# Kernel tuning notes

Hardware: AMD Instinct MI355X
Metric: run time of the kernel (lower is better)

## Reference

```python
import jax, jax.numpy as jnp
import numpy as np

NEG_INF = -1e10  # matches torch masked_fill value -10000000000.0


def setup_inputs() -> dict:
    key = jax.random.key(0)
    k1, k2, k3, k4 = jax.random.split(key, 4)
    B, Lq, Lk, D = 8, 2048, 2048, 1024
    hidden = jax.random.normal(k1, (B, Lq, D), dtype=jnp.float32)
    keys = jax.random.normal(k2, (B, Lk, D), dtype=jnp.float32)
    values = jax.random.normal(k3, (B, Lk, D), dtype=jnp.float32)
    mask = jax.random.randint(k4, (B, Lk), 0, 2, dtype=jnp.int32)
    return {"hidden": hidden, "keys": keys, "values": values, "mask": mask}


def reference(hidden, keys, values, mask):
    # scores[b,q,k] = sum_d hidden[b,q,d] * keys[b,k,d]  (unscaled dot-product)
    scores = jnp.einsum("bqd,bkd->bqk", hidden, keys)
    scores = jnp.where(mask[:, None, :] == 0, NEG_INF, scores)
    weights = jax.nn.softmax(scores, axis=2)  # (B, Lq, Lk)
    # context[b,q,d] = sum_k weights[b,q,k] * values[b,k,d]
    context = jnp.einsum("bqk,bkd->bqd", weights, values)
    return context
```

## Files before the change

### kernel.cpp

```cpp
#include <hip/hip_runtime.h>

#define NEG_INF -1e10f
#define B_   8
#define LQ_  2048
#define LK_  2048
#define D_   1024

typedef unsigned int uint;
typedef unsigned short u16;
typedef _Float16 f16;
typedef _Float16 f16x8_t __attribute__((ext_vector_type(8)));
typedef float f32x4_t __attribute__((ext_vector_type(4)));

__device__ __forceinline__ u16 f2h_bits(float f) {
    f16 h = (f16)f;
    return __builtin_bit_cast(u16, h);
}
__device__ __forceinline__ void gload_lds16(const void* g, void* l) {
    __builtin_amdgcn_global_load_lds(
        (const __attribute__((address_space(1))) uint*)g,
        (__attribute__((address_space(3))) uint*)l, 16, 0, 0);
}

__global__ __launch_bounds__(256) void convert_f16(
    const float4* __restrict__ src, ushort4* __restrict__ dst, int n4)
{
    int idx = blockIdx.x * 256 + threadIdx.x;
    const int stride = gridDim.x * 256;
    for (; idx < n4; idx += stride) {
        float4 x = src[idx];
        ushort4 h;
        h.x = f2h_bits(x.x);
        h.y = f2h_bits(x.y);
        h.z = f2h_bits(x.z);
        h.w = f2h_bits(x.w);
        dst[idx] = h;
    }
}

__global__ __launch_bounds__(256) void transpose_convert(
    const float* __restrict__ V, u16* __restrict__ VT)
{
    __shared__ float tile[64][65];
    const int t  = threadIdx.x;
    const int d0 = blockIdx.x * 64;
    const int k0 = blockIdx.y * 64;
    const float* Vb = V + (size_t)blockIdx.z * (LK_ * D_);
    u16* VTb = VT + (size_t)blockIdx.z * (D_ * LK_);
#pragma unroll
    for (int i = 0; i < 4; ++i) {
        int f = i * 256 + t;
        int r = f >> 4, c4 = f & 15;
        float4 v = *(const float4*)&Vb[(size_t)(k0 + r) * D_ + d0 + c4 * 4];
        tile[r][c4 * 4 + 0] = v.x;
        tile[r][c4 * 4 + 1] = v.y;
        tile[r][c4 * 4 + 2] = v.z;
        tile[r][c4 * 4 + 3] = v.w;
    }
    __syncthreads();
#pragma unroll
    for (int i = 0; i < 4; ++i) {
        int f = i * 256 + t;
        int d = f >> 4, c4 = f & 15;
        ushort4 o;
        o.x = f2h_bits(tile[c4 * 4 + 0][d]);
        o.y = f2h_bits(tile[c4 * 4 + 1][d]);
        o.z = f2h_bits(tile[c4 * 4 + 2][d]);
        o.w = f2h_bits(tile[c4 * 4 + 3][d]);
        *(ushort4*)&VTb[(size_t)(d0 + d) * LK_ + k0 + c4 * 4] = o;
    }
}

#define BM_  256
#define BK_  32

template<int NBF, int NTILES, bool SPLIT>
__global__ __launch_bounds__(512, 2) void gemm8p(
    const u16* __restrict__ A0g, const u16* __restrict__ A1g,
    const u16* __restrict__ Bg, float* __restrict__ Cg,
    int lda, int ldb, int ldc, int bkmask,
    size_t szA, size_t szB, size_t szC)
{
    constexpr int BN     = 64 * NBF;
    constexpr int ABYTES = BM_ * BK_ * 2;
    constexpr int BBYTES = BN * BK_ * 2;
    constexpr int BUFSZ  = ABYTES + BBYTES;
    __shared__ char lds[4 * BUFSZ];

    const int tid  = threadIdx.x;
    const int lane = tid & 63;
    const int w    = tid >> 6;
    const int wm   = w >> 2;
    const int wn   = w & 3;

    const int d  = blockIdx.x;
    const int g  = d & 7;
    const int k_ = d >> 3;
    const int by = (g >> 1) * 2 + (k_ & 1);
    const int bx = (g & 1) * 4 + (k_ >> 1);
    const int m0 = by * BM_;
    const int n0 = bx * BN;
    const size_t z = blockIdx.y;

    const u16* A0 = A0g + z * szA;
    const u16* A1 = A1g + z * szA;
    const u16* B  = Bg  + z * szB;
    float* C = Cg + z * szC;

    const int  lr   = lane & 15;
    const uint csel = (uint)((((lane >> 4) ^ ((lane >> 1) & 3)) * 16));
    const int  cstg = (((lane & 3) ^ ((lane >> 3) & 3)) * 8);
    const int  rstg = lane >> 2;

    const uint awoff = (uint)(wm * 8192 + lr * 64) + csel;
    const uint bwoff = (uint)(wn * (NBF * 1024) + lr * 64) + csel;

    f32x4_t acc[8][NBF];
#pragma unroll
    for (int m = 0; m < 8; ++m)
#pragma unroll
        for (int n = 0; n < NBF; ++n)
            acc[m][n] = (f32x4_t){0.f, 0.f, 0.f, 0.f};

    auto stA = [&](int t) {
        const u16* Ab;
        int kc;
        if constexpr (SPLIT) {
            Ab = (t < NTILES / 2) ? A0 : A1;
            kc = (t & (NTILES / 2 - 1)) * BK_ + cstg;
        } else {
            Ab = A0;
            kc = t * BK_ + cstg;
        }
        char* dst = lds + (t & 3) * BUFSZ + w * 2048;
        gload_lds16(&Ab[(size_t)(m0 + w * 32 + rstg) * lda + kc], dst);
        gload_lds16(&Ab[(size_t)(m0 + w * 32 + 16 + rstg) * lda + kc], dst + 1024);
    };
    auto stB = [&](int t) {
        const int kc = ((t * BK_) & bkmask) + cstg;
        char* dst = lds + (t & 3) * BUFSZ + ABYTES;
        if constexpr (NBF == 4) {
            gload_lds16(&B[(size_t)(n0 + w * 32 + rstg) * ldb + kc], dst + w * 2048);
            gload_lds16(&B[(size_t)(n0 + w * 32 + 16 + rstg) * ldb + kc], dst + w * 2048 + 1024);
        } else {
            gload_lds16(&B[(size_t)(n0 + w * 16 + rstg) * ldb + kc], dst + w * 1024);
        }
    };

    stA(0); stB(0); stA(1); stB(1); stA(2); stB(2);
    if constexpr (NBF == 4) asm volatile("s_waitcnt vmcnt(8)" ::: "memory");
    else                    asm volatile("s_waitcnt vmcnt(6)" ::: "memory");
    __builtin_amdgcn_s_barrier();

#define LDF(p) (*(const f16x8_t*)(p))

#define PHASE_A(T, DOSTAGE)                                                   \
    {                                                                         \
        const char* pA = lds + ((T) & 3) * BUFSZ + awoff;                     \
        const char* pB = lds + ((T) & 3) * BUFSZ + ABYTES + bwoff;            \
        f16x8_t a[4], b[NBF];                                                 \
        a[0] = LDF(pA);        a[1] = LDF(pA + 1024);                         \
        a[2] = LDF(pA + 2048); a[3] = LDF(pA + 3072);                         \
        b[0] = LDF(pB);                                                       \
        if constexpr (NBF >= 2) b[1] = LDF(pB + 1024);                        \
        if constexpr (NBF == 4) { b[2] = LDF(pB + 2048); b[3] = LDF(pB + 3072); } \
        if (DOSTAGE) stA((T) + 3);                                            \
        __builtin_amdgcn_s_barrier();                                         \
        __builtin_amdgcn_s_setprio(1);                                        \
        _Pragma("unroll")                                                     \
        for (int mf = 0; mf < 4; ++mf)                                        \
            _Pragma("unroll")                                                 \
            for (int nf = 0; nf < NBF; ++nf)                                  \
                acc[mf][nf] = __builtin_amdgcn_mfma_f32_16x16x32_f16(         \
                    a[mf], b[nf], acc[mf][nf], 0, 0, 0);                      \
        __builtin_amdgcn_s_setprio(0);                                        \
        bsave[0] = b[0];                                                      \
        if constexpr (NBF >= 2) bsave[1] = b[1];                              \
        if constexpr (NBF == 4) { bsave[2] = b[2]; bsave[3] = b[3]; }         \
        __builtin_amdgcn_s_barrier();                                         \
    }

#define PHASE_B(T, DOSTAGE, VMASM)                                            \
    {                                                                         \
        const char* pA = lds + ((T) & 3) * BUFSZ + awoff;                     \
        f16x8_t a[4];                                                         \
        a[0] = LDF(pA + 4096); a[1] = LDF(pA + 5120);                         \
        a[2] = LDF(pA + 6144); a[3] = LDF(pA + 7168);                         \
        if (DOSTAGE) stB((T) + 3);                                            \
        __builtin_amdgcn_s_barrier();                                         \
        __builtin_amdgcn_s_setprio(1);                                        \
        _Pragma("unroll")                                                     \
        for (int mf = 0; mf < 4; ++mf)                                        \
            _Pragma("unroll")                                                 \
            for (int nf = 0; nf < NBF; ++nf)                                  \
                acc[4 + mf][nf] = __builtin_amdgcn_mfma_f32_16x16x32_f16(     \
                    a[mf], bsave[nf], acc[4 + mf][nf], 0, 0, 0);              \
        __builtin_amdgcn_s_setprio(0);                                        \
        VMASM;                                                                \
        __builtin_amdgcn_s_barrier();                                         \
    }

#define VMW do { if constexpr (NBF == 4) asm volatile("s_waitcnt vmcnt(8)" ::: "memory"); \
                 else asm volatile("s_waitcnt vmcnt(6)" ::: "memory"); } while (0)
#define VMH do { if constexpr (NBF == 4) asm volatile("s_waitcnt vmcnt(4)" ::: "memory"); \
                 else asm volatile("s_waitcnt vmcnt(3)" ::: "memory"); } while (0)
#define VM0 asm volatile("s_waitcnt vmcnt(0)" ::: "memory")
#define VMN do {} while (0)

    f16x8_t bsave[NBF];

    for (int t = 0; t < NTILES - 3; ++t) {
        PHASE_A(t, true);
        PHASE_B(t, true, VMW);
    }
    PHASE_A(NTILES - 3, false); PHASE_B(NTILES - 3, false, VMH);
    PHASE_A(NTILES - 2, false); PHASE_B(NTILES - 2, false, VM0);
    PHASE_A(NTILES - 1, false); PHASE_B(NTILES - 1, false, VMN);
#undef PHASE_A
#undef PHASE_B
#undef LDF

    const int cg = lane >> 4;
#pragma unroll
    for (int mf = 0; mf < 8; ++mf)
#pragma unroll
        for (int nf = 0; nf < NBF; ++nf) {
            const int row = m0 + wm * 128 + mf * 16 + cg * 4;
            const int col = n0 + wn * (NBF * 16) + nf * 16 + lr;
#pragma unroll
            for (int r = 0; r < 4; ++r)
                C[(size_t)(row + r) * ldc + col] = acc[mf][nf][r];
        }
}

__global__ __launch_bounds__(256) void softmax_mask(
    float* __restrict__ S, const int* __restrict__ mask0)
{
    const int lane = threadIdx.x & 63;
    const int wave = threadIdx.x >> 6;
    const int row  = blockIdx.x * 4 + wave;
    const size_t zb = blockIdx.y;
    float* Sr = S + (zb * LQ_ + row) * (size_t)LK_;
    const int* mb = mask0 + zb * LK_;

    float4 s[8];
    float m = -INFINITY;
#pragma unroll
    for (int i = 0; i < 8; ++i) {
        int k = i * 256 + lane * 4;
        float4 v = *(const float4*)&Sr[k];
        int4 mk  = *(const int4*)&mb[k];
        v.x = mk.x ? v.x : NEG_INF;
        v.y = mk.y ? v.y : NEG_INF;
        v.z = mk.z ? v.z : NEG_INF;
        v.w = mk.w ? v.w : NEG_INF;
        s[i] = v;
        m = fmaxf(m, fmaxf(fmaxf(v.x, v.y), fmaxf(v.z, v.w)));
    }
#pragma unroll
    for (int off = 32; off > 0; off >>= 1)
        m = fmaxf(m, __shfl_xor(m, off, 64));
    float sum = 0.f;
#pragma unroll
    for (int i = 0; i < 8; ++i) {
        s[i].x = __expf(s[i].x - m); sum += s[i].x;
        s[i].y = __expf(s[i].y - m); sum += s[i].y;
        s[i].z = __expf(s[i].z - m); sum += s[i].z;
        s[i].w = __expf(s[i].w - m); sum += s[i].w;
    }
#pragma unroll
    for (int off = 32; off > 0; off >>= 1)
        sum += __shfl_xor(sum, off, 64);
    const float inv = 1.f / sum;
    u16* Pr = (u16*)Sr;
#pragma unroll
    for (int i = 0; i < 8; ++i) {
        int k = i * 256 + lane * 4;
        ushort4 o;
        o.x = f2h_bits(s[i].x * inv);
        o.y = f2h_bits(s[i].y * inv);
        o.z = f2h_bits(s[i].z * inv);
        o.w = f2h_bits(s[i].w * inv);
        *(ushort4*)&Pr[k] = o;
    }
}

__global__ __launch_bounds__(256, 2) void attn_fp32_flash(
    const float* __restrict__ hidden, const float* __restrict__ keys,
    const float* __restrict__ values, const int* __restrict__ mask,
    float* __restrict__ out)
{
    const int lane = threadIdx.x & 63;
    const int wave = threadIdx.x >> 6;
    const int blk  = blockIdx.x;
    const int b    = blk >> 7;
    const int q0   = (blk & 127) * 16 + wave * 4;
    float4 q[4][4]; float4 o[4][4]; float m[4], s[4];
    const float4* hp = (const float4*)(hidden + ((size_t)b * LQ_ + q0) * D_);
#pragma unroll
    for (int r = 0; r < 4; ++r) {
#pragma unroll
        for (int j = 0; j < 4; ++j) {
            q[r][j] = hp[r * 256 + j * 64 + lane];
            o[r][j] = make_float4(0.f, 0.f, 0.f, 0.f);
        }
        m[r] = -INFINITY; s[r] = 0.f;
    }
    const float4* kp = (const float4*)(keys   + (size_t)b * LK_ * D_);
    const float4* vp = (const float4*)(values + (size_t)b * LK_ * D_);
    const int*    mp = mask + b * LK_;
    for (int k = 0; k < LK_; ++k) {
        float4 kv[4];
#pragma unroll
        for (int j = 0; j < 4; ++j) kv[j] = kp[k * 256 + j * 64 + lane];
        float sc[4];
#pragma unroll
        for (int r = 0; r < 4; ++r) {
            float p = 0.f;
#pragma unroll
            for (int j = 0; j < 4; ++j)
                p += q[r][j].x * kv[j].x + q[r][j].y * kv[j].y +
                     q[r][j].z * kv[j].z + q[r][j].w * kv[j].w;
            sc[r] = p;
        }
#pragma unroll
        for (int r = 0; r < 4; ++r)
#pragma unroll
            for (int off = 32; off > 0; off >>= 1)
                sc[r] += __shfl_xor(sc[r], off, 64);
        const int mk = mp[k];
        float4 vv[4];
#pragma unroll
        for (int j = 0; j < 4; ++j) vv[j] = vp[k * 256 + j * 64 + lane];
#pragma unroll
        for (int r = 0; r < 4; ++r) {
            float score = mk ? sc[r] : NEG_INF;
            if (score > m[r]) {
                float scale = __expf(m[r] - score);
                m[r] = score; s[r] *= scale;
#pragma unroll
                for (int j = 0; j < 4; ++j) {
                    o[r][j].x *= scale; o[r][j].y *= scale;
                    o[r][j].z *= scale; o[r][j].w *= scale;
                }
            }
            float e = __expf(score - m[r]);
            s[r] += e;
#pragma unroll
            for (int j = 0; j < 4; ++j) {
                o[r][j].x += e * vv[j].x; o[r][j].y += e * vv[j].y;
                o[r][j].z += e * vv[j].z; o[r][j].w += e * vv[j].w;
            }
        }
    }
    float4* op = (float4*)(out + ((size_t)b * LQ_ + q0) * D_);
#pragma unroll
    for (int r = 0; r < 4; ++r) {
        float inv = 1.f / s[r];
#pragma unroll
        for (int j = 0; j < 4; ++j) {
            float4 t = o[r][j];
            t.x *= inv; t.y *= inv; t.z *= inv; t.w *= inv;
            op[r * 256 + j * 64 + lane] = t;
        }
    }
}

extern "C" void kernel_launch(void* const* d_in, const int* in_sizes, int n_in,
                              void* d_out, int out_size, void* d_ws, size_t ws_size,
                              hipStream_t stream) {
    const float* hidden = (const float*)d_in[0];
    const float* keys   = (const float*)d_in[1];
    const float* values = (const float*)d_in[2];
    const int*   mask   = (const int*)d_in[3];
    float* out = (float*)d_out;
    char* ws = (char*)d_ws;

    const size_t TEN = (size_t)LK_ * D_;
    const size_t MB  = 1024ull * 1024;

    int BG = 0;
    for (int g = 8; g >= 1; g >>= 1)
        if ((size_t)g * 28 * MB <= ws_size) { BG = g; break; }

    if (BG == 0) {
        attn_fp32_flash<<<1024, 256, 0, stream>>>(hidden, keys, values, mask, out);
        return;
    }

    const size_t SZ_BF = (size_t)BG * TEN * 2;
    u16*   Kh = (u16*)(ws);
    u16*   VT = (u16*)(ws + SZ_BF);
    u16*   Qh = (u16*)(ws + 2 * SZ_BF);
    float* S  = (float*)(ws + 3 * SZ_BF);

    const int n4 = BG * (int)(TEN / 4);

    for (int bg0 = 0; bg0 < B_; bg0 += BG) {
        const size_t off = (size_t)bg0 * TEN;
        convert_f16<<<2048, 256, 0, stream>>>(
            (const float4*)(keys + off), (ushort4*)Kh, n4);
        transpose_convert<<<dim3(16, 32, BG), 256, 0, stream>>>(
            values + off, VT);
        convert_f16<<<2048, 256, 0, stream>>>(
            (const float4*)(hidden + off), (ushort4*)Qh, n4);

        gemm8p<4, 32, false><<<dim3(64, BG), 512, 0, stream>>>(
            Qh, Qh, Kh, S, D_, D_, LK_, 1023,
            TEN, TEN, (size_t)LQ_ * LK_);

        softmax_mask<<<dim3(LQ_ / 4, BG), 256, 0, stream>>>(
            S, mask + bg0 * LK_);

        gemm8p<2, 64, true><<<dim3(64, BG), 512, 0, stream>>>(
            (const u16*)S, (const u16*)S + 1024, VT, out + off,
            2 * LK_, LK_, D_, 2047,
            (size_t)LQ_ * 2 * LK_, TEN, (size_t)LQ_ * D_);
    }
}
```

Measured before the change: 257.8 us.

## Widen PV GEMM tile to 256 columns and merge Q/K conversion launches

The second GEMM (weights times V^T) now uses NBF=4, giving 256-wide N tiles with 32 blocks per batch instead of 64, and the tile mapping for the split variant is adjusted to match. Each block reuses its A tile (the softmax weights) across more output columns, cutting LDS and global traffic for A. The two fp32-to-fp16 conversions for keys and hidden are fused into one launch to save a kernel launch. The trade-off is fewer blocks per batch, which lowers occupancy and parallelism on the GPU, and higher register use for accumulators.

After: 238.9 us. -7.3%, faster.

```diff
diff --git a/kernel.cpp b/kernel.cpp
--- a/kernel.cpp
+++ b/kernel.cpp
@@ -22,19 +22,22 @@
         (__attribute__((address_space(3))) uint*)l, 16, 0, 0);
 }
 
-__global__ __launch_bounds__(256) void convert_f16(
-    const float4* __restrict__ src, ushort4* __restrict__ dst, int n4)
+__global__ __launch_bounds__(256) void convert_f16_2(
+    const float4* __restrict__ s1, ushort4* __restrict__ d1,
+    const float4* __restrict__ s2, ushort4* __restrict__ d2, int n4)
 {
     int idx = blockIdx.x * 256 + threadIdx.x;
     const int stride = gridDim.x * 256;
-    for (; idx < n4; idx += stride) {
-        float4 x = src[idx];
+    for (; idx < 2 * n4; idx += stride) {
+        const bool second = idx >= n4;
+        const int i = second ? idx - n4 : idx;
+        float4 x = second ? s2[i] : s1[i];
         ushort4 h;
         h.x = f2h_bits(x.x);
         h.y = f2h_bits(x.y);
         h.z = f2h_bits(x.z);
         h.w = f2h_bits(x.w);
-        dst[idx] = h;
+        if (second) d2[i] = h; else d1[i] = h;
     }
 }
 
@@ -96,8 +99,14 @@
     const int d  = blockIdx.x;
     const int g  = d & 7;
     const int k_ = d >> 3;
-    const int by = (g >> 1) * 2 + (k_ & 1);
-    const int bx = (g & 1) * 4 + (k_ >> 1);
+    int by, bx;
+    if constexpr (!SPLIT) {
+        by = (g >> 1) * 2 + (k_ & 1);
+        bx = (g & 1) * 4 + (k_ >> 1);
+    } else {
+        by = (g >> 1) * 2 + (k_ & 1);
+        bx = (g & 1) * 2 + (k_ >> 1);
+    }
     const int m0 = by * BM_;
     const int n0 = bx * BN;
     const size_t z = blockIdx.y;
@@ -139,17 +148,12 @@
     auto stB = [&](int t) {
         const int kc = ((t * BK_) & bkmask) + cstg;
         char* dst = lds + (t & 3) * BUFSZ + ABYTES;
-        if constexpr (NBF == 4) {
-            gload_lds16(&B[(size_t)(n0 + w * 32 + rstg) * ldb + kc], dst + w * 2048);
-            gload_lds16(&B[(size_t)(n0 + w * 32 + 16 + rstg) * ldb + kc], dst + w * 2048 + 1024);
-        } else {
-            gload_lds16(&B[(size_t)(n0 + w * 16 + rstg) * ldb + kc], dst + w * 1024);
-        }
+        gload_lds16(&B[(size_t)(n0 + w * 32 + rstg) * ldb + kc], dst + w * 2048);
+        gload_lds16(&B[(size_t)(n0 + w * 32 + 16 + rstg) * ldb + kc], dst + w * 2048 + 1024);
     };
 
     stA(0); stB(0); stA(1); stB(1); stA(2); stB(2);
-    if constexpr (NBF == 4) asm volatile("s_waitcnt vmcnt(8)" ::: "memory");
-    else                    asm volatile("s_waitcnt vmcnt(6)" ::: "memory");
+    asm volatile("s_waitcnt vmcnt(8)" ::: "memory");
     __builtin_amdgcn_s_barrier();
 
 #define LDF(p) (*(const f16x8_t*)(p))
@@ -161,9 +165,8 @@
         f16x8_t a[4], b[NBF];                                                 \
         a[0] = LDF(pA);        a[1] = LDF(pA + 1024);                         \
         a[2] = LDF(pA + 2048); a[3] = LDF(pA + 3072);                         \
-        b[0] = LDF(pB);                                                       \
-        if constexpr (NBF >= 2) b[1] = LDF(pB + 1024);                        \
-        if constexpr (NBF == 4) { b[2] = LDF(pB + 2048); b[3] = LDF(pB + 3072); } \
+        b[0] = LDF(pB);        b[1] = LDF(pB + 1024);                         \
+        b[2] = LDF(pB + 2048); b[3] = LDF(pB + 3072);                         \
         if (DOSTAGE) stA((T) + 3);                                            \
         __builtin_amdgcn_s_barrier();                                         \
         __builtin_amdgcn_s_setprio(1);                                        \
@@ -174,9 +177,7 @@
                 acc[mf][nf] = __builtin_amdgcn_mfma_f32_16x16x32_f16(         \
                     a[mf], b[nf], acc[mf][nf], 0, 0, 0);                      \
         __builtin_amdgcn_s_setprio(0);                                        \
-        bsave[0] = b[0];                                                      \
-        if constexpr (NBF >= 2) bsave[1] = b[1];                              \
-        if constexpr (NBF == 4) { bsave[2] = b[2]; bsave[3] = b[3]; }         \
+        bsave[0] = b[0]; bsave[1] = b[1]; bsave[2] = b[2]; bsave[3] = b[3];   \
         __builtin_amdgcn_s_barrier();                                         \
     }
 
@@ -200,10 +201,8 @@
         __builtin_amdgcn_s_barrier();                                         \
     }
 
-#define VMW do { if constexpr (NBF == 4) asm volatile("s_waitcnt vmcnt(8)" ::: "memory"); \
-                 else asm volatile("s_waitcnt vmcnt(6)" ::: "memory"); } while (0)
-#define VMH do { if constexpr (NBF == 4) asm volatile("s_waitcnt vmcnt(4)" ::: "memory"); \
-                 else asm volatile("s_waitcnt vmcnt(3)" ::: "memory"); } while (0)
+#define VMW asm volatile("s_waitcnt vmcnt(8)" ::: "memory")
+#define VMH asm volatile("s_waitcnt vmcnt(4)" ::: "memory")
 #define VM0 asm volatile("s_waitcnt vmcnt(0)" ::: "memory")
 #define VMN do {} while (0)
 
@@ -398,12 +397,11 @@
 
     for (int bg0 = 0; bg0 < B_; bg0 += BG) {
         const size_t off = (size_t)bg0 * TEN;
-        convert_f16<<<2048, 256, 0, stream>>>(
-            (const float4*)(keys + off), (ushort4*)Kh, n4);
+        convert_f16_2<<<4096, 256, 0, stream>>>(
+            (const float4*)(keys + off), (ushort4*)Kh,
+            (const float4*)(hidden + off), (ushort4*)Qh, n4);
         transpose_convert<<<dim3(16, 32, BG), 256, 0, stream>>>(
             values + off, VT);
-        convert_f16<<<2048, 256, 0, stream>>>(
-            (const float4*)(hidden + off), (ushort4*)Qh, n4);
 
         gemm8p<4, 32, false><<<dim3(64, BG), 512, 0, stream>>>(
             Qh, Qh, Kh, S, D_, D_, LK_, 1023,
@@ -412,7 +410,7 @@
         softmax_mask<<<dim3(LQ_ / 4, BG), 256, 0, stream>>>(
             S, mask + bg0 * LK_);
 
-        gemm8p<2, 64, true><<<dim3(64, BG), 512, 0, stream>>>(
+        gemm8p<4, 64, true><<<dim3(32, BG), 512, 0, stream>>>(
             (const u16*)S, (const u16*)S + 1024, VT, out + off,
             2 * LK_, LK_, D_, 2047,
             (size_t)LQ_ * 2 * LK_, TEN, (size_t)LQ_ * D_);
```
